# Kernel tuning notes

Hardware: AMD Instinct MI355X
Metric: run time of the kernel (lower is better)

The kernel has to match this reference:

```python
import jax, jax.numpy as jnp
import numpy as np

KSIZE = 7
LOSS_WEIGHT = 1.0


def _box_filter(x, ksize):
    # x: (N, 1, H, W) already reflect-padded -> valid conv with ones kernel
    kern = jnp.ones((1, 1, ksize, ksize), x.dtype)
    return jax.lax.conv_general_dilated(
        x, kern, window_strides=(1, 1), padding='VALID',
        dimension_numbers=('NCHW', 'OIHW', 'NCHW'))


def _local_var(residual, ksize):
    # unbiased variance over each ksize x ksize window (reflect padding),
    # computed via box-filtered sum and sum-of-squares (same math as
    # torch.var over unfolded windows, without materializing the windows).
    pad = (ksize - 1) // 2
    rp = jnp.pad(residual, ((0, 0), (0, 0), (pad, pad), (pad, pad)), mode='reflect')
    n = ksize * ksize
    s = _box_filter(rp, ksize)        # window sums
    ss = _box_filter(rp * rp, ksize)  # window sums of squares
    return (ss - s * s / n) / (n - 1)


def setup_inputs() -> dict:
    key = jax.random.key(0)
    k1, k2 = jax.random.split(key)
    shape = (16, 3, 512, 512)
    pred = jax.random.normal(k1, shape, dtype=jnp.float32)
    target = jax.random.normal(k2, shape, dtype=jnp.float32)
    return {"pred": pred, "target": target}


def reference(pred, target):
    # residual over channels: (N, 1, H, W)
    residual = jnp.sum(jnp.abs(target - pred), axis=1, keepdims=True)
    # patch-level weight: unbiased var over (C,H,W), ^(1/5)
    patch_w = jnp.var(residual, axis=(1, 2, 3), keepdims=True, ddof=1) ** 0.2
    # pixel-level weight: local unbiased variance in ksize window
    pixel_w = _local_var(residual, KSIZE)
    overall_weight = patch_w * pixel_w  # (N, 1, H, W), broadcasts over C
    # L1 criterion on weighted pred vs weighted target
    return jnp.mean(jnp.abs(overall_weight * pred - overall_weight * target)) * LOSS_WEIGHT
```

## Files before the change

kernel.cpp:

```cpp
#include <hip/hip_runtime.h>
#include <math.h>

#define N_IMG 16
#define C_CH 3
#define H_DIM 512
#define W_DIM 512
#define HW (H_DIM * W_DIM)
#define KS 7
#define PAD 3

#define TS 64
#define TILE (TS + 2 * PAD)
#define TSTRIDE 72
#define TPB 256
#define TILES_PER_IMG ((H_DIM / TS) * (W_DIM / TS))
#define NBLOCKS (N_IMG * TILES_PER_IMG)


__global__ __launch_bounds__(TPB) void k_fused(const float* __restrict__ pred,
                                               const float* __restrict__ targ,
                                               float* __restrict__ pr,
                                               float* __restrict__ pr2,
                                               float* __restrict__ pc) {
    __shared__ float tile[TILE * TSTRIDE];

    const int bid = blockIdx.x;
    const int n   = bid >> 6;
    const int t   = bid & 63;
    const int by  = t >> 3;
    const int bx  = t & 7;
    const int tid = threadIdx.x;

    const float* p0 = pred + (size_t)n * C_CH * HW;
    const float* p1 = p0 + HW;
    const float* p2 = p1 + HW;
    const float* q0 = targ + (size_t)n * C_CH * HW;
    const float* q1 = q0 + HW;
    const float* q2 = q1 + HW;

    const int y0 = by * TS - PAD;
    const int x0 = bx * TS - PAD;
#pragma unroll 4
    for (int it = 0; it < 19; ++it) {
        const int i  = tid + it * TPB;
        const int ly = i / TILE;
        const int lx = i - ly * TILE;
        int gy = y0 + ly;
        int gx = x0 + lx;
        gy = (gy < 0) ? -gy : ((gy >= H_DIM) ? (2 * H_DIM - 2 - gy) : gy);
        gx = (gx < 0) ? -gx : ((gx >= W_DIM) ? (2 * W_DIM - 2 - gx) : gx);
        const int off = gy * W_DIM + gx;
        tile[ly * TSTRIDE + lx] = fabsf(q0[off] - p0[off])
                                + fabsf(q1[off] - p1[off])
                                + fabsf(q2[off] - p2[off]);
    }
    if (tid < 36) {
        const int i  = tid + 19 * TPB;
        const int ly = i / TILE;
        const int lx = i - ly * TILE;
        int gy = y0 + ly;
        int gx = x0 + lx;
        gy = (gy < 0) ? -gy : ((gy >= H_DIM) ? (2 * H_DIM - 2 - gy) : gy);
        gx = (gx < 0) ? -gx : ((gx >= W_DIM) ? (2 * W_DIM - 2 - gx) : gx);
        const int off = gy * W_DIM + gx;
        tile[ly * TSTRIDE + lx] = fabsf(q0[off] - p0[off])
                                + fabsf(q1[off] - p1[off])
                                + fabsf(q2[off] - p2[off]);
    }
    __syncthreads();

    const int tx  = tid & 63;
    const int ty0 = (tid >> 6) << 4;

    float rS[KS], rSS[KS];
    float S = 0.f, SS = 0.f;
#pragma unroll
    for (int dy = 0; dy < KS; ++dy) {
        float s = 0.f, ss = 0.f;
#pragma unroll
        for (int j = 0; j < KS; ++j) {
            const float v = tile[(ty0 + dy) * TSTRIDE + tx + j];
            s  += v;
            ss += v * v;
        }
        rS[dy] = s; rSS[dy] = ss;
        S += s; SS += ss;
    }

    float acc_r = 0.f, acc_r2 = 0.f, acc_c = 0.f;

#pragma unroll
    for (int k = 0; k < 16; ++k) {
        if (k > 0) {
            float s = 0.f, ss = 0.f;
#pragma unroll
            for (int j = 0; j < KS; ++j) {
                const float v = tile[(ty0 + 6 + k) * TSTRIDE + tx + j];
                s  += v;
                ss += v * v;
            }
            const int slot = (k - 1) % KS;
            S  += s  - rS[slot];
            SS += ss - rSS[slot];
            rS[slot] = s; rSS[slot] = ss;
        }
        const float pix_var = (SS - S * S * (1.0f / 49.0f)) * (1.0f / 48.0f);
        const float center  = tile[(ty0 + 3 + k) * TSTRIDE + tx + 3];

        acc_r  += center;
        acc_r2 += center * center;
        acc_c  += pix_var * center;
    }

#pragma unroll
    for (int off = 32; off > 0; off >>= 1) {
        acc_r  += __shfl_down(acc_r,  off);
        acc_r2 += __shfl_down(acc_r2, off);
        acc_c  += __shfl_down(acc_c,  off);
    }
    __shared__ float sh_r[4], sh_r2[4], sh_c[4];
    const int lane = tid & 63;
    const int wave = tid >> 6;
    if (lane == 0) { sh_r[wave] = acc_r; sh_r2[wave] = acc_r2; sh_c[wave] = acc_c; }
    __syncthreads();
    if (tid == 0) {
        pr [bid] = sh_r [0] + sh_r [1] + sh_r [2] + sh_r [3];
        pr2[bid] = sh_r2[0] + sh_r2[1] + sh_r2[2] + sh_r2[3];
        pc [bid] = sh_c [0] + sh_c [1] + sh_c [2] + sh_c [3];
    }
}

__global__ void k_final(const float* __restrict__ pr,
                        const float* __restrict__ pr2,
                        const float* __restrict__ pc,
                        float* __restrict__ out) {
    __shared__ double sh[N_IMG];
    const int tid  = threadIdx.x;
    const int w    = tid >> 6;
    const int lane = tid & 63;

    double R = 0.0, R2 = 0.0, Cs = 0.0;
    if (lane < TILES_PER_IMG) {
        const int idx = w * TILES_PER_IMG + lane;
        R  = (double)pr[idx];
        R2 = (double)pr2[idx];
        Cs = (double)pc[idx];
    }
#pragma unroll
    for (int off = 32; off > 0; off >>= 1) {
        R  += __shfl_down(R,  off);
        R2 += __shfl_down(R2, off);
        Cs += __shfl_down(Cs, off);
    }
    if (lane == 0) {
        const double pvar = (R2 - R * R / (double)HW) / (double)(HW - 1);
        sh[w] = pow(pvar, 0.2) * Cs;
    }
    __syncthreads();
    if (tid == 0) {
        double s = 0.0;
        for (int i = 0; i < N_IMG; ++i) s += sh[i];
        out[0] = (float)(s / ((double)N_IMG * C_CH * HW));
    }
}

extern "C" void kernel_launch(void* const* d_in, const int* in_sizes, int n_in,
                              void* d_out, int out_size, void* d_ws, size_t ws_size,
                              hipStream_t stream) {
    const float* pred = (const float*)d_in[0];
    const float* targ = (const float*)d_in[1];

    float* pr  = (float*)d_ws;
    float* pr2 = pr  + NBLOCKS;
    float* pc  = pr2 + NBLOCKS;
    float* out = (float*)d_out;

    k_fused<<<NBLOCKS, TPB, 0, stream>>>(pred, targ, pr, pr2, pc);
    k_final<<<1, 1024, 0, stream>>>(pr, pr2, pc, out);
}
```

Baseline: 127.9 us.

## Fuse final reduction into main kernel via last-block atomic counter and remap block order

Removes the separate single-block finalize kernel by having each block increment an atomic counter after writing its partials, with the last block performing the per-image variance and final reduction. It also permutes block indices so consecutive hardware block IDs are spread across images and tiles, likely to spread work across the XCDs or memory channels. A memset launch is added to reset the counter, so launch count stays the same. The last block's serial tail and the fence and atomic overhead remain.

```diff
diff --git a/kernel.cpp b/kernel.cpp
--- a/kernel.cpp
+++ b/kernel.cpp
@@ -21,10 +21,12 @@
                                                const float* __restrict__ targ,
                                                float* __restrict__ pr,
                                                float* __restrict__ pr2,
-                                               float* __restrict__ pc) {
+                                               float* __restrict__ pc,
+                                               int* __restrict__ cnt,
+                                               float* __restrict__ out) {
     __shared__ float tile[TILE * TSTRIDE];
 
-    const int bid = blockIdx.x;
+    const int bid = ((blockIdx.x & 7) << 7) | (blockIdx.x >> 3);
     const int n   = bid >> 6;
     const int t   = bid & 63;
     const int by  = t >> 3;
@@ -123,44 +125,45 @@
     const int wave = tid >> 6;
     if (lane == 0) { sh_r[wave] = acc_r; sh_r2[wave] = acc_r2; sh_c[wave] = acc_c; }
     __syncthreads();
+
+    __shared__ int s_last;
     if (tid == 0) {
         pr [bid] = sh_r [0] + sh_r [1] + sh_r [2] + sh_r [3];
         pr2[bid] = sh_r2[0] + sh_r2[1] + sh_r2[2] + sh_r2[3];
         pc [bid] = sh_c [0] + sh_c [1] + sh_c [2] + sh_c [3];
-    }
-}
-
-__global__ void k_final(const float* __restrict__ pr,
-                        const float* __restrict__ pr2,
-                        const float* __restrict__ pc,
-                        float* __restrict__ out) {
-    __shared__ double sh[N_IMG];
-    const int tid  = threadIdx.x;
-    const int w    = tid >> 6;
-    const int lane = tid & 63;
-
-    double R = 0.0, R2 = 0.0, Cs = 0.0;
-    if (lane < TILES_PER_IMG) {
-        const int idx = w * TILES_PER_IMG + lane;
-        R  = (double)pr[idx];
-        R2 = (double)pr2[idx];
-        Cs = (double)pc[idx];
-    }
-#pragma unroll
-    for (int off = 32; off > 0; off >>= 1) {
-        R  += __shfl_down(R,  off);
-        R2 += __shfl_down(R2, off);
-        Cs += __shfl_down(Cs, off);
-    }
-    if (lane == 0) {
-        const double pvar = (R2 - R * R / (double)HW) / (double)(HW - 1);
-        sh[w] = pow(pvar, 0.2) * Cs;
+        __threadfence();
+        const int old = atomicAdd(cnt, 1);
+        s_last = (old == NBLOCKS - 1);
     }
     __syncthreads();
-    if (tid == 0) {
-        double s = 0.0;
-        for (int i = 0; i < N_IMG; ++i) s += sh[i];
-        out[0] = (float)(s / ((double)N_IMG * C_CH * HW));
+
+    if (s_last) {
+        __threadfence();
+        __shared__ double sh[N_IMG];
+#pragma unroll
+        for (int i = 0; i < 4; ++i) {
+            const int img = wave * 4 + i;
+            const int idx = img * TILES_PER_IMG + lane;
+            double R  = (double)pr [idx];
+            double R2 = (double)pr2[idx];
+            double Cs = (double)pc [idx];
+#pragma unroll
+            for (int off = 32; off > 0; off >>= 1) {
+                R  += __shfl_down(R,  off);
+                R2 += __shfl_down(R2, off);
+                Cs += __shfl_down(Cs, off);
+            }
+            if (lane == 0) {
+                const double pvar = (R2 - R * R / (double)HW) / (double)(HW - 1);
+                sh[img] = pow(pvar, 0.2) * Cs;
+            }
+        }
+        __syncthreads();
+        if (tid == 0) {
+            double s = 0.0;
+            for (int i = 0; i < N_IMG; ++i) s += sh[i];
+            out[0] = (float)(s / ((double)N_IMG * C_CH * HW));
+        }
     }
 }
 
@@ -173,8 +176,9 @@
     float* pr  = (float*)d_ws;
     float* pr2 = pr  + NBLOCKS;
     float* pc  = pr2 + NBLOCKS;
+    int*   cnt = (int*)(pc + NBLOCKS);
     float* out = (float*)d_out;
 
-    k_fused<<<NBLOCKS, TPB, 0, stream>>>(pred, targ, pr, pr2, pc);
-    k_final<<<1, 1024, 0, stream>>>(pr, pr2, pc, out);
+    hipMemsetAsync(cnt, 0, sizeof(int), stream);
+    k_fused<<<NBLOCKS, TPB, 0, stream>>>(pred, targ, pr, pr2, pc, cnt, out);
 }
```

Result: slower. 173.4 us (+35.5%).
